# Kernel optimization log

Measured on AMD Instinct MI355X. Metric: run time of the kernel, lower is better.

## Reference

```python
import jax, jax.numpy as jnp
import numpy as np
from jax import lax

BIG = jnp.float32(1e8)  # stand-in for +inf (no zeros found yet)
EPS_W = 1e-3
SMOOTH = 1e-6
ALPHA = 0.6
BETA = 1.0


def _scan_dist(zmask):
    # zmask: (H, B, W) bool, True where pixel == 0.
    # Forward 1D chamfer pass along leading axis: exact 1D distance to nearest zero.
    def body(c, z):
        d = jnp.where(z, jnp.float32(0.0), c + jnp.float32(1.0))
        return d, d
    init = jnp.full(zmask.shape[1:], BIG, jnp.float32)
    _, out = lax.scan(body, init, zmask)
    return out  # (H, B, W)


def edt(t):
    # Exact Euclidean distance transform (distance to nearest zero), t: (B, H, W).
    # Separable Felzenszwalb-style: exact 1D pass along H, then lower-envelope
    # (brute-force min via scan) along W on squared distances.
    z = (t == 0)
    zm = jnp.moveaxis(z, 1, 0)                      # (H, B, W)
    fwd = _scan_dist(zm)
    bwd = _scan_dist(zm[::-1])[::-1]
    d1 = jnp.minimum(fwd, bwd)                      # 1D distance along H
    g = jnp.minimum(d1 * d1, BIG)                   # squared, (H, B, W)

    W = g.shape[-1]
    ys = jnp.arange(W, dtype=jnp.float32)
    g_cols = jnp.moveaxis(g, 2, 0)                  # (W, H, B)

    def body2(carry, xs):
        gcol, j = xs                                # gcol: (H, B)
        cand = gcol[..., None] + (ys - j) ** 2      # (H, B, W)
        return jnp.minimum(carry, cand), None

    init = jnp.full(g.shape, BIG, jnp.float32)
    out, _ = lax.scan(body2, init, (g_cols, ys))    # (H, B, W) squared EDT
    return jnp.sqrt(jnp.moveaxis(out, 1, 0))        # (B, H, W)


def setup_inputs() -> dict:
    key = jax.random.key(0)
    k1, k2 = jax.random.split(key)
    B, C, H, W = 16, 1, 512, 512
    inputs = jax.random.normal(k1, (B, C, H, W), dtype=jnp.float32)
    targets = jax.random.randint(k2, (B, C, H, W), 0, 2).astype(jnp.float32)
    return {"inputs": inputs, "targets": targets}


def reference(inputs, targets):
    B = targets.shape[0]
    t2d = targets[:, 0]                             # (B, H, W), squeeze channel
    w_edt = edt(t2d)                                # per-sample EDT, (B, H, W)
    v = jnp.max(w_edt, axis=(1, 2))                 # scalar max per sample
    # Faithful to original (buggy) indexing: w = v - w_edt[b] (row b, shape (W,))
    rows = w_edt[jnp.arange(B), jnp.arange(B), :]   # (B, W)
    mask = (w_edt != 0).astype(jnp.float32)         # (B, H, W)
    w = mask * (v[:, None, None] - rows[:, None, :]) + jnp.float32(EPS_W)
    weight = lax.stop_gradient(w)[:, None, :, :]    # (B, 1, H, W); no grad (numpy in orig)

    wmse = jnp.mean(weight * (inputs - targets) ** 2)

    p = jax.nn.sigmoid(inputs).reshape(-1)
    tg = targets.reshape(-1)
    intersection = jnp.sum(p * tg)
    union = jnp.sum(p) + jnp.sum(tg)
    dice = 1.0 - (2.0 * intersection + SMOOTH) / (union + SMOOTH)

    return (ALPHA * wmse, BETA * dice)
```

## Files before the change

### kernel.cpp

```cpp
#include <hip/hip_runtime.h>

#define W      512
#define IMG    (512 * 512)
#define NB     16
#define NPIX   (NB * IMG)

#define TILE_H 16
#define APRON  8
#define LROWS  (TILE_H + 2 * APRON)
#define BLOCK  1024
#define GRID   (NB * (W / TILE_H))

struct WS {
    unsigned int vmax[16];
    float C[16 * 512];
    float rows[16 * 512];
    float4 partial[GRID];
};

__device__ __forceinline__ unsigned pk_min_u16(unsigned a, unsigned b) {
    unsigned r; asm("v_pk_min_u16 %0, %1, %2" : "=v"(r) : "v"(a), "v"(b)); return r;
}
__device__ __forceinline__ unsigned pk_max_u16(unsigned a, unsigned b) {
    unsigned r; asm("v_pk_max_u16 %0, %1, %2" : "=v"(r) : "v"(a), "v"(b)); return r;
}

__device__ int exact_best(const float* __restrict__ img, int h, int y) {
    int best = 100000000;
    for (int gh = 0; gh < W; ++gh) {
        int dhh = gh - h;
        if (dhh * dhh >= best) continue;
        const float* rp = img + (gh << 9);
        for (int yy = 0; yy < W; ++yy)
            if (rp[yy] == 0.0f) {
                int dx = yy - y;
                best = min(best, dhh * dhh + dx * dx);
            }
    }
    return best;
}

__global__ __launch_bounds__(BLOCK, 8) void fused_kernel(const float* __restrict__ inp,
                                                         const float* __restrict__ tgt,
                                                         WS* __restrict__ ws) {
    __shared__ union {
        struct {
            unsigned long long zm[LROWS][10];
            unsigned short Dd[LROWS][W];
            unsigned int smax[BLOCK / 64];
        } e;
        struct {
            float4 csh[8][128];
            float4 ssum[BLOCK / 64];
        } l;
    } sh;

    int bid  = blockIdx.x;
    int b    = bid >> 5;
    int tile = bid & 31;
    int h0   = tile * TILE_H;
    int tid  = threadIdx.x;
    int wave = tid >> 6, lane = tid & 63;
    const float* img = tgt + (size_t)b * IMG;

    size_t base4 = (size_t)b * (IMG / 4) + (size_t)tile * (TILE_H * W / 4);
    const float4* x4 = (const float4*)inp + base4;
    const float4* t4 = (const float4*)tgt + base4;

    float s0 = 0.f, s1 = 0.f, s2 = 0.f, s3 = 0.f;
    float4 ct = make_float4(0.f, 0.f, 0.f, 0.f);
    #pragma unroll
    for (int k = 0; k < 2; ++k) {
        int i = tid + (k << 10);
        float4 xv = x4[i];
        float4 tv = t4[i];
        { float d = xv.x - tv.x; float e2 = d * d; s0 += e2; ct.x += tv.x * e2;
          float p = 1.0f / (1.0f + __expf(-xv.x)); s1 += p * tv.x; s2 += p; s3 += tv.x; }
        { float d = xv.y - tv.y; float e2 = d * d; s0 += e2; ct.y += tv.y * e2;
          float p = 1.0f / (1.0f + __expf(-xv.y)); s1 += p * tv.y; s2 += p; s3 += tv.y; }
        { float d = xv.z - tv.z; float e2 = d * d; s0 += e2; ct.z += tv.z * e2;
          float p = 1.0f / (1.0f + __expf(-xv.z)); s1 += p * tv.z; s2 += p; s3 += tv.z; }
        { float d = xv.w - tv.w; float e2 = d * d; s0 += e2; ct.w += tv.w * e2;
          float p = 1.0f / (1.0f + __expf(-xv.w)); s1 += p * tv.w; s2 += p; s3 += tv.w; }
    }
    sh.l.csh[tid >> 7][tid & 127] = ct;
    #pragma unroll
    for (int o = 32; o > 0; o >>= 1) {
        s0 += __shfl_down(s0, o); s1 += __shfl_down(s1, o);
        s2 += __shfl_down(s2, o); s3 += __shfl_down(s3, o);
    }
    if (lane == 0) sh.l.ssum[wave] = make_float4(s0, s1, s2, s3);
    __syncthreads();

    if (tid < 128) {
        float4 a = sh.l.csh[0][tid];
        #pragma unroll
        for (int g = 1; g < 8; ++g) {
            float4 c = sh.l.csh[g][tid];
            a.x += c.x; a.y += c.y; a.z += c.z; a.w += c.w;
        }
        float* Cb = ws->C + (b << 9) + (tid << 2);
        atomicAdd(Cb + 0, a.x);
        atomicAdd(Cb + 1, a.y);
        atomicAdd(Cb + 2, a.z);
        atomicAdd(Cb + 3, a.w);
    } else if (tid == 128) {
        float4 a = sh.l.ssum[0];
        #pragma unroll
        for (int i = 1; i < BLOCK / 64; ++i) {
            a.x += sh.l.ssum[i].x; a.y += sh.l.ssum[i].y;
            a.z += sh.l.ssum[i].z; a.w += sh.l.ssum[i].w;
        }
        ws->partial[bid] = a;
    }
    __syncthreads();

    auto& zm = sh.e.zm;
    auto& Dd = sh.e.Dd;
    for (int wi = wave; wi < LROWS * 8; wi += BLOCK / 64) {
        int lr = wi >> 3, wc = wi & 7;
        int gh = h0 - APRON + lr;
        unsigned long long m = 0ULL;
        if (gh >= 0 && gh < W) {
            float v = img[(gh << 9) + (wc << 6) + lane];
            m = __ballot(v == 0.0f);
        }
        if (lane == 0) zm[lr][wc + 1] = m;
    }
    if (tid < LROWS) { zm[tid][0] = 0ULL; zm[tid][9] = 0ULL; }
    __syncthreads();

    for (int u = wave; u < LROWS * 8; u += BLOCK / 64) {
        int lr = u >> 3, wc = u & 7;
        unsigned long long Wm = zm[lr][wc];
        unsigned long long Wc = zm[lr][wc + 1];
        unsigned long long Wp = zm[lr][wc + 2];
        int off = lane;
        unsigned long long wr = (Wc >> off) | (off ? (Wp << (64 - off)) : 0ULL);
        int dr = wr ? __builtin_ctzll(wr) : 1000;
        unsigned long long vl = off ? ((Wc << (64 - off)) | (Wm >> off)) : Wm;
        int dl = vl ? (1 + __builtin_clzll(vl)) : 1000;
        int d = min(min(dr, dl), 1000);
        int dd = min(d * d, 65471);
        Dd[lr][(wc << 6) + lane] = (unsigned short)dd;
    }
    __syncthreads();

    int p = tid & 255;
    int q = tid >> 8;
    const unsigned* Dd32 = (const unsigned*)&Dd[0][0];
    const unsigned* basep = Dd32 + (q << 10) + p;
    unsigned col[20];
    #pragma unroll
    for (int j = 0; j < 20; ++j) col[j] = basep[j * 256];

    unsigned best[4];
    #pragma unroll
    for (int m = 0; m < 4; ++m) {
        unsigned bb = 0xFFFFFFFFu;
        #pragma unroll
        for (int j = 0; j <= 16; ++j) {
            unsigned dh2 = (unsigned)((j - 8) * (j - 8));
            bb = pk_min_u16(bb, col[m + j] + dh2 * 0x00010001u);
        }
        best[m] = bb;
    }
    unsigned bpk = pk_max_u16(pk_max_u16(best[0], best[1]), pk_max_u16(best[2], best[3]));
    unsigned tmax = max(bpk & 0xFFFFu, bpk >> 16);

    if (__builtin_expect(tmax > 81u, 0)) {
        tmax = 0;
        for (int m = 0; m < 4; ++m) {
            int k = (q << 2) + m;
            unsigned nb = 0;
            for (int half = 0; half < 2; ++half) {
                int y = (p << 1) + half;
                int bb = 1 << 30;
                for (int j = 0; j <= 16; ++j)
                    bb = min(bb, (j - 8) * (j - 8) + (int)Dd[k + j][y]);
                if (bb > 81) bb = exact_best(img, h0 + k, y);
                tmax = max(tmax, (unsigned)bb);
                nb |= ((unsigned)bb & 0xFFFFu) << (half * 16);
            }
            best[m] = nb;
        }
    }

    if (tile == 0 && q == (b >> 2)) {
        unsigned rb = best[b & 3];
        ws->rows[(b << 9) + (p << 1)]     = sqrtf((float)(rb & 0xFFFFu));
        ws->rows[(b << 9) + (p << 1) + 1] = sqrtf((float)(rb >> 16));
    }

    #pragma unroll
    for (int o = 32; o > 0; o >>= 1) tmax = max(tmax, (unsigned)__shfl_down(tmax, o));
    if (lane == 0) sh.e.smax[wave] = tmax;
    __syncthreads();
    if (tid == 0) {
        unsigned bm = sh.e.smax[0];
        #pragma unroll
        for (int i = 1; i < BLOCK / 64; ++i) bm = max(bm, sh.e.smax[i]);
        atomicMax(&ws->vmax[b], bm);
    }
}

#define FBLOCK 256
__global__ __launch_bounds__(FBLOCK) void final_kernel(const WS* __restrict__ ws,
                                                       float* __restrict__ out) {
    int tid = threadIdx.x;
    __shared__ float vsh[16];
    if (tid < 16) vsh[tid] = sqrtf((float)ws->vmax[tid]);
    __syncthreads();

    double wm = 0.0;
    #pragma unroll
    for (int j = 0; j < (16 * 512) / FBLOCK; ++j) {
        int cell = tid + j * FBLOCK;
        wm += (double)ws->C[cell] * (double)(vsh[cell >> 9] - ws->rows[cell]);
    }
    double e = 0, s1 = 0, s2 = 0, s3 = 0;
    #pragma unroll
    for (int j = 0; j < GRID / FBLOCK; ++j) {
        float4 p = ws->partial[tid + j * FBLOCK];
        e += p.x; s1 += p.y; s2 += p.z; s3 += p.w;
    }

    #pragma unroll
    for (int o = 32; o > 0; o >>= 1) {
        wm += __shfl_down(wm, o); e  += __shfl_down(e, o);
        s1 += __shfl_down(s1, o); s2 += __shfl_down(s2, o); s3 += __shfl_down(s3, o);
    }
    __shared__ double shd[FBLOCK / 64][5];
    int lane = tid & 63, wid = tid >> 6;
    if (lane == 0) { shd[wid][0] = wm; shd[wid][1] = e;
                     shd[wid][2] = s1; shd[wid][3] = s2; shd[wid][4] = s3; }
    __syncthreads();
    if (tid == 0) {
        double a0 = 0, a1 = 0, a2 = 0, a3 = 0, a4 = 0;
        #pragma unroll
        for (int i = 0; i < FBLOCK / 64; ++i) {
            a0 += shd[i][0]; a1 += shd[i][1]; a2 += shd[i][2]; a3 += shd[i][3]; a4 += shd[i][4];
        }
        double wmse = (a0 + 0.001 * a1) / (double)NPIX;
        out[0] = (float)(0.6 * wmse);
        out[1] = (float)(1.0 - (2.0 * a2 + 1e-6) / (a3 + a4 + 1e-6));
    }
}

extern "C" void kernel_launch(void* const* d_in, const int* in_sizes, int n_in,
                              void* d_out, int out_size, void* d_ws, size_t ws_size,
                              hipStream_t stream) {
    const float* inp = (const float*)d_in[0];
    const float* tgt = (const float*)d_in[1];
    float* out = (float*)d_out;
    WS* ws = (WS*)d_ws;

    hipMemsetAsync(d_ws, 0, sizeof(unsigned int) * 16 + sizeof(float) * 16 * 512, stream);
    fused_kernel<<<GRID, BLOCK, 0, stream>>>(inp, tgt, ws);
    final_kernel<<<1, FBLOCK, 0, stream>>>(ws, out);
}
```

Baseline: 96.90 us.

## Fuse final reduction into main kernel via last-block counter and drop shared union

Removes the separate final reduction kernel launch: each block increments a global counter after a threadfence, and the last block to finish performs the final weighted-MSE and dice reduction. The shared-memory union is split into separate arrays, so the loss-partial reduction can move after the first barrier and one __syncthreads is dropped. This saves a kernel launch and one barrier, but raises per-block LDS use, which may lower occupancy, and adds a serial tail in the last block.

```diff
diff --git a/kernel.cpp b/kernel.cpp
--- a/kernel.cpp
+++ b/kernel.cpp
@@ -13,10 +13,13 @@
 
 struct WS {
     unsigned int vmax[16];
-    float C[16 * 512];
-    float rows[16 * 512];
+    float C[NB * W];
+    unsigned int counter;
+    unsigned int pad[7];
+    float rows[NB * W];
     float4 partial[GRID];
 };
+#define MEMSET_BYTES (sizeof(unsigned int) * 16 + sizeof(float) * NB * W + sizeof(unsigned int))
 
 __device__ __forceinline__ unsigned pk_min_u16(unsigned a, unsigned b) {
     unsigned r; asm("v_pk_min_u16 %0, %1, %2" : "=v"(r) : "v"(a), "v"(b)); return r;
@@ -42,18 +45,16 @@
 
 __global__ __launch_bounds__(BLOCK, 8) void fused_kernel(const float* __restrict__ inp,
                                                          const float* __restrict__ tgt,
-                                                         WS* __restrict__ ws) {
-    __shared__ union {
-        struct {
-            unsigned long long zm[LROWS][10];
-            unsigned short Dd[LROWS][W];
-            unsigned int smax[BLOCK / 64];
-        } e;
-        struct {
-            float4 csh[8][128];
-            float4 ssum[BLOCK / 64];
-        } l;
-    } sh;
+                                                         WS* __restrict__ ws,
+                                                         float* __restrict__ out) {
+    __shared__ unsigned long long zm[LROWS][10];
+    __shared__ unsigned short Dd[LROWS][W];
+    __shared__ float4 csh[8][128];
+    __shared__ float4 ssum[BLOCK / 64];
+    __shared__ unsigned smax[BLOCK / 64];
+    __shared__ double shd[BLOCK / 64][5];
+    __shared__ float vsh[16];
+    __shared__ int sh_last;
 
     int bid  = blockIdx.x;
     int b    = bid >> 5;
@@ -83,40 +84,14 @@
         { float d = xv.w - tv.w; float e2 = d * d; s0 += e2; ct.w += tv.w * e2;
           float p = 1.0f / (1.0f + __expf(-xv.w)); s1 += p * tv.w; s2 += p; s3 += tv.w; }
     }
-    sh.l.csh[tid >> 7][tid & 127] = ct;
+    csh[tid >> 7][tid & 127] = ct;
     #pragma unroll
     for (int o = 32; o > 0; o >>= 1) {
         s0 += __shfl_down(s0, o); s1 += __shfl_down(s1, o);
         s2 += __shfl_down(s2, o); s3 += __shfl_down(s3, o);
     }
-    if (lane == 0) sh.l.ssum[wave] = make_float4(s0, s1, s2, s3);
-    __syncthreads();
-
-    if (tid < 128) {
-        float4 a = sh.l.csh[0][tid];
-        #pragma unroll
-        for (int g = 1; g < 8; ++g) {
-            float4 c = sh.l.csh[g][tid];
-            a.x += c.x; a.y += c.y; a.z += c.z; a.w += c.w;
-        }
-        float* Cb = ws->C + (b << 9) + (tid << 2);
-        atomicAdd(Cb + 0, a.x);
-        atomicAdd(Cb + 1, a.y);
-        atomicAdd(Cb + 2, a.z);
-        atomicAdd(Cb + 3, a.w);
-    } else if (tid == 128) {
-        float4 a = sh.l.ssum[0];
-        #pragma unroll
-        for (int i = 1; i < BLOCK / 64; ++i) {
-            a.x += sh.l.ssum[i].x; a.y += sh.l.ssum[i].y;
-            a.z += sh.l.ssum[i].z; a.w += sh.l.ssum[i].w;
-        }
-        ws->partial[bid] = a;
-    }
-    __syncthreads();
-
-    auto& zm = sh.e.zm;
-    auto& Dd = sh.e.Dd;
+    if (lane == 0) ssum[wave] = make_float4(s0, s1, s2, s3);
+
     for (int wi = wave; wi < LROWS * 8; wi += BLOCK / 64) {
         int lr = wi >> 3, wc = wi & 7;
         int gh = h0 - APRON + lr;
@@ -129,6 +104,27 @@
     }
     if (tid < LROWS) { zm[tid][0] = 0ULL; zm[tid][9] = 0ULL; }
     __syncthreads();
+
+    if (tid < 128) {
+        float4 a = csh[0][tid];
+        #pragma unroll
+        for (int g = 1; g < 8; ++g) {
+            float4 c = csh[g][tid];
+            a.x += c.x; a.y += c.y; a.z += c.z; a.w += c.w;
+        }
+        float* Cb = ws->C + (b << 9) + (tid << 2);
+        atomicAdd(Cb + 0, a.x);
+        atomicAdd(Cb + 1, a.y);
+        atomicAdd(Cb + 2, a.z);
+        atomicAdd(Cb + 3, a.w);
+    } else if (tid == 128) {
+        float4 a = ssum[0];
+        #pragma unroll
+        for (int i = 1; i < BLOCK / 64; ++i) {
+            a.x += ssum[i].x; a.y += ssum[i].y; a.z += ssum[i].z; a.w += ssum[i].w;
+        }
+        ws->partial[bid] = a;
+    }
 
     for (int u = wave; u < LROWS * 8; u += BLOCK / 64) {
         int lr = u >> 3, wc = u & 7;
@@ -194,51 +190,54 @@
 
     #pragma unroll
     for (int o = 32; o > 0; o >>= 1) tmax = max(tmax, (unsigned)__shfl_down(tmax, o));
-    if (lane == 0) sh.e.smax[wave] = tmax;
+    if (lane == 0) smax[wave] = tmax;
     __syncthreads();
     if (tid == 0) {
-        unsigned bm = sh.e.smax[0];
-        #pragma unroll
-        for (int i = 1; i < BLOCK / 64; ++i) bm = max(bm, sh.e.smax[i]);
+        unsigned bm = smax[0];
+        #pragma unroll
+        for (int i = 1; i < BLOCK / 64; ++i) bm = max(bm, smax[i]);
         atomicMax(&ws->vmax[b], bm);
     }
-}
-
-#define FBLOCK 256
-__global__ __launch_bounds__(FBLOCK) void final_kernel(const WS* __restrict__ ws,
-                                                       float* __restrict__ out) {
-    int tid = threadIdx.x;
-    __shared__ float vsh[16];
-    if (tid < 16) vsh[tid] = sqrtf((float)ws->vmax[tid]);
+
+    __threadfence();
+    __syncthreads();
+    if (tid == 0) {
+        unsigned old = atomicAdd(&ws->counter, 1u);
+        sh_last = (old == GRID - 1);
+    }
+    __syncthreads();
+    if (!sh_last) return;
+    __threadfence();
+
+    if (tid < 16) vsh[tid] = sqrtf((float)((volatile unsigned*)ws->vmax)[tid]);
     __syncthreads();
 
     double wm = 0.0;
     #pragma unroll
-    for (int j = 0; j < (16 * 512) / FBLOCK; ++j) {
-        int cell = tid + j * FBLOCK;
-        wm += (double)ws->C[cell] * (double)(vsh[cell >> 9] - ws->rows[cell]);
-    }
-    double e = 0, s1 = 0, s2 = 0, s3 = 0;
-    #pragma unroll
-    for (int j = 0; j < GRID / FBLOCK; ++j) {
-        float4 p = ws->partial[tid + j * FBLOCK];
-        e += p.x; s1 += p.y; s2 += p.z; s3 += p.w;
+    for (int j = 0; j < (NB * W) / BLOCK; ++j) {
+        int cell = tid + (j << 10);
+        float c = ((volatile float*)ws->C)[cell];
+        float r = ((volatile float*)ws->rows)[cell];
+        wm += (double)c * (double)(vsh[cell >> 9] - r);
+    }
+    double e = 0, t1 = 0, t2 = 0, t3 = 0;
+    if (tid < GRID) {
+        volatile float* pp = (volatile float*)&ws->partial[tid];
+        e = pp[0]; t1 = pp[1]; t2 = pp[2]; t3 = pp[3];
     }
 
     #pragma unroll
     for (int o = 32; o > 0; o >>= 1) {
         wm += __shfl_down(wm, o); e  += __shfl_down(e, o);
-        s1 += __shfl_down(s1, o); s2 += __shfl_down(s2, o); s3 += __shfl_down(s3, o);
-    }
-    __shared__ double shd[FBLOCK / 64][5];
-    int lane = tid & 63, wid = tid >> 6;
-    if (lane == 0) { shd[wid][0] = wm; shd[wid][1] = e;
-                     shd[wid][2] = s1; shd[wid][3] = s2; shd[wid][4] = s3; }
+        t1 += __shfl_down(t1, o); t2 += __shfl_down(t2, o); t3 += __shfl_down(t3, o);
+    }
+    if (lane == 0) { shd[wave][0] = wm; shd[wave][1] = e;
+                     shd[wave][2] = t1; shd[wave][3] = t2; shd[wave][4] = t3; }
     __syncthreads();
     if (tid == 0) {
         double a0 = 0, a1 = 0, a2 = 0, a3 = 0, a4 = 0;
         #pragma unroll
-        for (int i = 0; i < FBLOCK / 64; ++i) {
+        for (int i = 0; i < BLOCK / 64; ++i) {
             a0 += shd[i][0]; a1 += shd[i][1]; a2 += shd[i][2]; a3 += shd[i][3]; a4 += shd[i][4];
         }
         double wmse = (a0 + 0.001 * a1) / (double)NPIX;
@@ -255,7 +254,6 @@
     float* out = (float*)d_out;
     WS* ws = (WS*)d_ws;
 
-    hipMemsetAsync(d_ws, 0, sizeof(unsigned int) * 16 + sizeof(float) * 16 * 512, stream);
-    fused_kernel<<<GRID, BLOCK, 0, stream>>>(inp, tgt, ws);
-    final_kernel<<<1, FBLOCK, 0, stream>>>(ws, out);
-}
+    hipMemsetAsync(d_ws, 0, MEMSET_BYTES, stream);
+    fused_kernel<<<GRID, BLOCK, 0, stream>>>(inp, tgt, ws, out);
+}
```

New measurement: 213.6 us. 120% more time.
